# Optimization experiments

Hardware: AMD Instinct MI355X
Metric: run time of the kernel (lower is better)

The kernel has to match this reference:

```python
import jax, jax.numpy as jnp
import numpy as np

V, C, L, D = 16384, 16, 6, 64  # n_vars, max_clauses, max_variables, embedding_dim


def _normalize(x):
    # utils.normalize: L2-normalize along the feature axis
    return x / jnp.linalg.norm(x, axis=-1, keepdims=True)


def _rescombine(x, W1, b1, W2, b2):
    # ResidualCombine: normalize(sigmoid(layer1(x)) + layer2(x))
    h = jax.nn.sigmoid(x @ W1 + b1) + x @ W2 + b2
    return _normalize(h)


def setup_inputs() -> dict:
    key = jax.random.key(0)
    ks = jax.random.split(key, 14)
    s = 0.05
    variables = jax.random.normal(ks[0], (V, D), jnp.float32)
    # literal variable indices; slot 0 of every clause is the owning variable i
    lits = jax.random.randint(ks[1], (V, C, L), 0, V)
    lits = lits.at[:, :, 0].set(jnp.arange(V)[:, None])
    neg_mask = jax.random.bernoulli(ks[2], 0.5, (V, C, L))
    # literal validity: at least 2 literals per clause, slot 0 always valid
    nvar = jax.random.randint(ks[3], (V, C), 2, L + 1)
    var_valid = jnp.arange(L)[None, None, :] < nvar[:, :, None]
    # clause validity: at least 1 clause per variable
    nclause = jax.random.randint(ks[4], (V,), 1, C + 1)
    clause_valid = jnp.arange(C)[None, :] < nclause[:, None]
    # params
    Wn = jax.random.normal(ks[5], (D, D), jnp.float32) * s
    bn = jnp.zeros((D,), jnp.float32)
    f = jax.random.normal(ks[6], (D,), jnp.float32)
    false_emb = f / jnp.linalg.norm(f)  # Embedding(1, D, max_norm=1.0)
    W1v = jax.random.normal(ks[7], (L * D, D), jnp.float32) * s
    b1v = jnp.zeros((D,), jnp.float32)
    W2v = jax.random.normal(ks[8], (L * D, D), jnp.float32) * s
    b2v = jnp.zeros((D,), jnp.float32)
    W1c = jax.random.normal(ks[9], (C * D, D), jnp.float32) * s
    b1c = jnp.zeros((D,), jnp.float32)
    W2c = jax.random.normal(ks[10], (C * D, D), jnp.float32) * s
    b2c = jnp.zeros((D,), jnp.float32)
    return dict(variables=variables, lits=lits, neg_mask=neg_mask, var_valid=var_valid,
                clause_valid=clause_valid, Wn=Wn, bn=bn, false_emb=false_emb,
                W1v=W1v, b1v=b1v, W2v=W2v, b2v=b2v, W1c=W1c, b1c=b1c, W2c=W2c, b2c=b2c)


def reference(variables, lits, neg_mask, var_valid, clause_valid,
              Wn, bn, false_emb, W1v, b1v, W2v, b2v, W1c, b1c, W2c, b2c):
    # gather literal embeddings: [V, C, L, D]
    g = variables[lits]
    # negation linear for negative literals
    v = jnp.where(neg_mask[..., None], g @ Wn + bn, g)
    # pad invalid literal slots with the 'false' embedding
    v = jnp.where(var_valid[..., None], v, false_emb)
    # variable_combiner over flattened [L*D]
    clause_emb = _rescombine(v.reshape(V, C, L * D), W1v, b1v, W2v, b2v)  # [V, C, D]
    # pad missing clauses with 'true' = negation(false)
    true_emb = false_emb @ Wn + bn
    clause_emb = jnp.where(clause_valid[..., None], clause_emb, true_emb)
    # clause_combiner over flattened [C*D]
    out = _rescombine(clause_emb.reshape(V, C * D), W1c, b1c, W2c, b2c)  # [V, D]
    # variables with no clauses pass through unchanged
    has_clauses = clause_valid.any(axis=-1)
    return jnp.where(has_clauses[:, None], out, variables)
```

## Files before the change

### kernel.cpp

```cpp
#include <hip/hip_runtime.h>
#include <hip/hip_bf16.h>

#define NV 16384
#define NC 16
#define NL 6
#define ND 64

typedef unsigned short u16;
typedef unsigned int u32;
typedef __attribute__((ext_vector_type(8))) short short8;
typedef __attribute__((ext_vector_type(4))) float f32x4;

#define PB_BN  0
#define PB_FE  64
#define PB_B1V 128
#define PB_B2V 192
#define PB_B1C 256
#define PB_B2C 320
#define U_BVS   896
#define U_BCS   50048
#define U_VARSB 185216
#define U_NEGB  1233856
#define U_FIDX  2282496

__device__ __forceinline__ float ldbf(const u16* p, int i) {
  return __uint_as_float(((u32)p[i]) << 16);
}
__device__ __forceinline__ u16 f2b(float f) {
  u32 x = __float_as_uint(f);
  return (u16)((x + 0x7FFF + ((x >> 16) & 1)) >> 16);
}
__device__ __forceinline__ int ldmask(const void* p, int i, int bdt) {
  return bdt ? (int)((const signed char*)p)[i] : ((const int*)p)[i];
}
__device__ __forceinline__ float ldf(const void* p, int i, int fdt) {
  return fdt ? ldbf((const u16*)p, i) : ((const float*)p)[i];
}
__device__ __forceinline__ void gll16(const u16* g, u16* l) {
  __builtin_amdgcn_global_load_lds(
      (const __attribute__((address_space(1))) u32*)(g),
      (__attribute__((address_space(3))) u32*)(l), 16, 0, 0);
}

__global__ __launch_bounds__(256) void k_prep(
    const void* vars, const int* __restrict__ lits, const void* negm, const void* vval,
    const void* Wn, const void* bn, const void* femb,
    const void* W1v, const void* b1v, const void* W2v, const void* b2v,
    const void* W1c, const void* b1c, const void* W2c, const void* b2c,
    int* flags, float* pbuf, u16* wsB) {
  __shared__ int s_cnt[4], s_big[4];
  __shared__ __align__(16) u16 BnL[4096];
  const int t = threadIdx.x;
  {
    const u32 w = ((const u32*)vars)[t];
    const u32 e = (w >> 7) & 0xFF;
    const unsigned long long bal = __ballot(e >= 0x6E && e <= 0x8E);
    const u32 bw = ((const u32*)vval)[t];
    const unsigned long long bb = __ballot(bw > 1u);
    if ((t & 63) == 0) { s_cnt[t >> 6] = __popcll(bal); s_big[t >> 6] = (bb != 0ull); }
  }
  __syncthreads();
  const int fdt = (s_cnt[0] + s_cnt[1] + s_cnt[2] + s_cnt[3]) >= 192;
  const int bdt = (s_big[0] | s_big[1] | s_big[2] | s_big[3]);
  const int bid = blockIdx.x;

  if (bid == 0) {
    if (t == 0) { flags[0] = fdt; flags[1] = bdt; }
    if (t < 64) {
      const void* src[6] = {bn, femb, b1v, b2v, b1c, b2c};
      const int off[6] = {PB_BN, PB_FE, PB_B1V, PB_B2V, PB_B1C, PB_B2C};
      for (int j = 0; j < 6; j++) pbuf[off[j] + t] = ldf(src[j], t, fdt);
      wsB[U_VARSB + NV * 64 + t] = fdt ? ((const u16*)femb)[t] : f2b(((const float*)femb)[t]);
    }
  } else if (bid < 25) {
    const int c = (bid - 1) * 256 + t;
    const int ln = c & 63, nt = (c >> 6) & 7, ks = c >> 9;
    const int n = nt * 16 + (ln & 15);
    const void* src = (n < 64) ? W1v : W2v;
    const int kb = ks * 32 + (ln >> 4) * 8, n6 = n & 63;
    u16 o[8];
#pragma unroll
    for (int j = 0; j < 8; j++) o[j] = f2b(ldf(src, (kb + j) * 64 + n6, fdt));
    *(short8*)(wsB + U_BVS + c * 8) = *(short8*)o;
  } else if (bid < 89) {
    const int c = (bid - 25) * 256 + t;
    const int ln = c & 63, nt = (c >> 6) & 7, ks = c >> 9;
    const int n = nt * 16 + (ln & 15);
    const void* src = (n < 64) ? W1c : W2c;
    const int kb = ks * 32 + (ln >> 4) * 8, n6 = n & 63;
    u16 o[8];
#pragma unroll
    for (int j = 0; j < 8; j++) o[j] = f2b(ldf(src, (kb + j) * 64 + n6, fdt));
    *(short8*)(wsB + U_BCS + c * 8) = *(short8*)o;
  } else if (bid < 217) {
    const int c8 = ((bid - 89) * 256 + t) * 4;
#pragma unroll
    for (int cc = 0; cc < 4; cc++) {
      u16 o[8];
      if (fdt) {
        *(short8*)o = ((const short8*)vars)[c8 + cc];
      } else {
        const float* f = (const float*)vars + (c8 + cc) * 8;
#pragma unroll
        for (int j = 0; j < 8; j++) o[j] = f2b(f[j]);
      }
      *(short8*)(wsB + U_VARSB + (c8 + cc) * 8) = *(short8*)o;
    }
  } else if (bid < 601) {
    const int i0 = ((bid - 217) * 256 + t) * 16;
    u16 o[16];
    if (!bdt) {
      const int4* lp = (const int4*)(lits + i0);
      const int4* vp = (const int4*)((const int*)vval + i0);
      const int4* np = (const int4*)((const int*)negm + i0);
#pragma unroll
      for (int c4 = 0; c4 < 4; c4++) {
        const int4 L = lp[c4], V = vp[c4], N = np[c4];
        o[c4 * 4 + 0] = (u16)(V.x ? (L.x + (N.x ? (NV + 1) : 0)) : NV);
        o[c4 * 4 + 1] = (u16)(V.y ? (L.y + (N.y ? (NV + 1) : 0)) : NV);
        o[c4 * 4 + 2] = (u16)(V.z ? (L.z + (N.z ? (NV + 1) : 0)) : NV);
        o[c4 * 4 + 3] = (u16)(V.w ? (L.w + (N.w ? (NV + 1) : 0)) : NV);
      }
    } else {
#pragma unroll
      for (int j = 0; j < 16; j++) {
        const int i = i0 + j;
        const int valid = ldmask(vval, i, bdt);
        const int neg = ldmask(negm, i, bdt);
        o[j] = (u16)(valid ? (lits[i] + (neg ? (NV + 1) : 0)) : NV);
      }
    }
    *(short8*)(wsB + U_FIDX + i0) = *(short8*)o;
    *(short8*)(wsB + U_FIDX + i0 + 8) = *(short8*)(o + 8);
  } else {
    const int lane = t & 63, wv = t >> 6;
    const int col = lane & 15, quad = lane >> 4, q8 = quad * 8;
    const int rowbase = (bid - 601) * 64 + wv * 16;
    for (int i = t; i < 4096; i += 256) {
      const int n = i >> 6, k = i & 63;
      BnL[i] = f2b(ldf(Wn, k * 64 + n, fdt));
    }
    __syncthreads();
    const int arow = min(rowbase + col, NV);
    short8 a[2];
    if (fdt) {
      const u16* src = (arow == NV) ? (const u16*)femb : (const u16*)vars + arow * 64;
      a[0] = *(const short8*)(src + q8);
      a[1] = *(const short8*)(src + 32 + q8);
    } else {
      const float* src = (arow == NV) ? (const float*)femb : (const float*)vars + arow * 64;
      u16 tmp[16];
#pragma unroll
      for (int j = 0; j < 8; j++) tmp[j] = f2b(src[q8 + j]);
#pragma unroll
      for (int j = 0; j < 8; j++) tmp[8 + j] = f2b(src[32 + q8 + j]);
      a[0] = *(short8*)tmp;
      a[1] = *(short8*)(tmp + 8);
    }
    f32x4 acc[4];
#pragma unroll
    for (int nt = 0; nt < 4; nt++) acc[nt] = (f32x4){0.f, 0.f, 0.f, 0.f};
#pragma unroll
    for (int ks = 0; ks < 2; ks++) {
#pragma unroll
      for (int nt = 0; nt < 4; nt++) {
        const short8 b = *(const short8*)(BnL + (nt * 16 + col) * 64 + ks * 32 + q8);
        acc[nt] = __builtin_amdgcn_mfma_f32_16x16x32_bf16(a[ks], b, acc[nt], 0, 0, 0);
      }
    }
#pragma unroll
    for (int reg = 0; reg < 4; reg++) {
      const int r = rowbase + quad * 4 + reg;
      if (r <= NV) {
#pragma unroll
        for (int nt = 0; nt < 4; nt++) {
          const int d = nt * 16 + col;
          wsB[U_NEGB + r * 64 + d] = f2b(acc[nt][reg] + ldf(bn, d, fdt));
        }
      }
    }
  }
}

__global__ __launch_bounds__(256, 2) void k_main(
    const void* __restrict__ vars, const void* __restrict__ cval,
    const float* __restrict__ pbuf, const int* __restrict__ flags,
    const u16* __restrict__ wsB, void* __restrict__ outv) {
  __shared__ __align__(16) u16 smem[24576];
  __shared__ float ps[16][4];
  __shared__ int hcS[16];

  const int tid = threadIdx.x, lane = tid & 63, wv = tid >> 6;
  const int col = lane & 15, quad = lane >> 4, q8 = quad * 8;
  const int fdt = flags[0], bdt = flags[1];
  const int vbase = (blockIdx.x * 4 + wv) * 4;
  const int v0 = blockIdx.x * 16;

  u32 r2_[4][3];
#pragma unroll
  for (int v4 = 0; v4 < 4; v4++)
#pragma unroll
    for (int i = 0; i < 3; i++)
      r2_[v4][i] = *(const u32*)(wsB + U_FIDX + (vbase + v4) * 96 + col * 6 + i * 2);

  const int cv = ldmask(cval, vbase * 16 + lane, bdt);
  const unsigned long long bal = __ballot(cv != 0);
  if (lane < 4) hcS[wv * 4 + lane] = ((bal >> (lane * 16)) & 0xFFFFull) != 0;

  f32x4 acc[4][8];
#pragma unroll
  for (int v4 = 0; v4 < 4; v4++)
#pragma unroll
    for (int nt = 0; nt < 8; nt++) acc[v4][nt] = (f32x4){0.f, 0.f, 0.f, 0.f};

#pragma unroll
  for (int j = 0; j < 6; j++) {
    const int cl = wv * 6 + j;
    gll16(wsB + U_BVS + cl * 512 + lane * 8, &smem[cl * 512]);
  }
  short8 a_cur[4], a_nxt[4];
#pragma unroll
  for (int v4 = 0; v4 < 4; v4++) {
    const int idx = (int)(r2_[v4][0] & 0xFFFFu);
    a_cur[v4] = *(const short8*)(wsB + U_VARSB + idx * 64 + q8);
  }
  __syncthreads();

  for (int q = 0; q < 4; q++) {
    if (q < 3) {
#pragma unroll
      for (int j = 0; j < 6; j++) {
        const int cl = wv * 6 + j;
        gll16(wsB + U_BVS + (q + 1) * 12288 + cl * 512 + lane * 8,
              &smem[((q + 1) & 1) * 12288 + cl * 512]);
      }
    }
#pragma unroll
    for (int ksl = 0; ksl < 3; ksl++) {
      const int gk = q * 3 + ksl;
      if (gk < 11) {
        const int gn = gk + 1;
        const int goff = (gn & 1) * 32 + q8;
        const int pi = gn >> 2, ph = (gn >> 1) & 1;
#pragma unroll
        for (int v4 = 0; v4 < 4; v4++) {
          const int idx = (int)((r2_[v4][pi] >> (ph * 16)) & 0xFFFFu);
          a_nxt[v4] = *(const short8*)(wsB + U_VARSB + idx * 64 + goff);
        }
      }
#pragma unroll
      for (int nt = 0; nt < 8; nt++) {
        const short8 b = *(const short8*)(&smem[(q & 1) * 12288 + (ksl * 8 + nt) * 512 + lane * 8]);
#pragma unroll
        for (int v4 = 0; v4 < 4; v4++)
          acc[v4][nt] = __builtin_amdgcn_mfma_f32_16x16x32_bf16(a_cur[v4], b, acc[v4][nt], 0, 0, 0);
      }
#pragma unroll
      for (int v4 = 0; v4 < 4; v4++) a_cur[v4] = a_nxt[v4];
    }
    if (q < 3) __syncthreads();
  }
  __syncthreads();

  {
    float b1l[4], b2l[4], truel[4];
#pragma unroll
    for (int nt = 0; nt < 4; nt++) {
      const int d = nt * 16 + col;
      b1l[nt] = pbuf[PB_B1V + d];
      b2l[nt] = pbuf[PB_B2V + d];
      truel[nt] = ldbf(wsB, U_NEGB + NV * 64 + d);
    }
#pragma unroll
    for (int v4 = 0; v4 < 4; v4++) {
      const u32 vmask = (u32)((bal >> (v4 * 16)) & 0xFFFFull);
      const int vloc = wv * 4 + v4;
#pragma unroll
      for (int reg = 0; reg < 4; reg++) {
        const int c = quad * 4 + reg;
        float hh[4], ss = 0.f;
#pragma unroll
        for (int nt = 0; nt < 4; nt++) {
          hh[nt] = 1.0f / (1.0f + __expf(-(acc[v4][nt][reg] + b1l[nt]))) + acc[v4][nt + 4][reg] + b2l[nt];
          ss += hh[nt] * hh[nt];
        }
        ss += __shfl_xor(ss, 1, 64); ss += __shfl_xor(ss, 2, 64);
        ss += __shfl_xor(ss, 4, 64); ss += __shfl_xor(ss, 8, 64);
        const float sc = 1.0f / sqrtf(ss);
        const int valid = (vmask >> c) & 1;
#pragma unroll
        for (int nt = 0; nt < 4; nt++) {
          const float o = valid ? hh[nt] * sc : truel[nt];
          const int l2 = (nt * 2 + (col >> 3)) & 3;
          smem[(c * 2 + (nt >> 1)) * 512 + (l2 * 16 + vloc) * 8 + (col & 7)] = f2b(o);
        }
      }
    }
  }
  __syncthreads();

  f32x4 acc1 = (f32x4){0.f, 0.f, 0.f, 0.f}, acc2 = (f32x4){0.f, 0.f, 0.f, 0.f};
#pragma unroll 8
  for (int ks = 0; ks < 32; ks++) {
    const short8 a = *(const short8*)(&smem[ks * 512 + lane * 8]);
    const short8 b1 = *(const short8*)(wsB + U_BCS + (ks * 8 + wv) * 512 + lane * 8);
    const short8 b2 = *(const short8*)(wsB + U_BCS + (ks * 8 + wv + 4) * 512 + lane * 8);
    acc1 = __builtin_amdgcn_mfma_f32_16x16x32_bf16(a, b1, acc1, 0, 0, 0);
    acc2 = __builtin_amdgcn_mfma_f32_16x16x32_bf16(a, b2, acc2, 0, 0, 0);
  }

  const int d = wv * 16 + col;
  const float b1c_d = pbuf[PB_B1C + d], b2c_d = pbuf[PB_B2C + d];
  float h[4];
#pragma unroll
  for (int reg = 0; reg < 4; reg++) {
    h[reg] = 1.0f / (1.0f + __expf(-(acc1[reg] + b1c_d))) + acc2[reg] + b2c_d;
    float ssp = h[reg] * h[reg];
    ssp += __shfl_xor(ssp, 1, 64); ssp += __shfl_xor(ssp, 2, 64);
    ssp += __shfl_xor(ssp, 4, 64); ssp += __shfl_xor(ssp, 8, 64);
    if (col == 0) ps[quad * 4 + reg][wv] = ssp;
  }
  __syncthreads();
#pragma unroll
  for (int reg = 0; reg < 4; reg++) {
    const int r = quad * 4 + reg;
    const float tot = ps[r][0] + ps[r][1] + ps[r][2] + ps[r][3];
    float o = h[reg] * (1.0f / sqrtf(tot));
    const int oi = (v0 + r) * 64 + d;
    if (hcS[r]) {
      if (fdt) ((u16*)outv)[oi] = f2b(o);
      else ((float*)outv)[oi] = o;
    } else {
      if (fdt) ((u16*)outv)[oi] = ((const u16*)vars)[oi];
      else ((float*)outv)[oi] = ((const float*)vars)[oi];
    }
  }
}

extern "C" void kernel_launch(void* const* d_in, const int* in_sizes, int n_in,
                              void* d_out, int out_size, void* d_ws, size_t ws_size,
                              hipStream_t stream) {
  const void* vars = d_in[0];
  const int* lits = (const int*)d_in[1];
  const void* negm = d_in[2];
  const void* vval = d_in[3];
  const void* cvalid = d_in[4];
  const void* Wn = d_in[5];
  const void* bn = d_in[6];
  const void* femb = d_in[7];
  const void* W1v = d_in[8];
  const void* b1v = d_in[9];
  const void* W2v = d_in[10];
  const void* b2v = d_in[11];
  const void* W1c = d_in[12];
  const void* b1c = d_in[13];
  const void* W2c = d_in[14];
  const void* b2c = d_in[15];

  int* flags = (int*)d_ws;
  float* pbuf = (float*)((char*)d_ws + 256);
  u16* wsB = (u16*)d_ws;

  k_prep<<<858, 256, 0, stream>>>(vars, lits, negm, vval, Wn, bn, femb,
                                  W1v, b1v, W2v, b2v, W1c, b1c, W2c, b2c,
                                  flags, pbuf, wsB);
  k_main<<<NV / 16, 256, 0, stream>>>(vars, cvalid, pbuf, flags, wsB, d_out);
}
```

Baseline: 159.4 us.

## Double k_main block to 32 variables with 8 waves and reuse clause weights

```diff
diff --git a/kernel.cpp b/kernel.cpp
--- a/kernel.cpp
+++ b/kernel.cpp
@@ -75,9 +75,9 @@
   } else if (bid < 25) {
     const int c = (bid - 1) * 256 + t;
     const int ln = c & 63, nt = (c >> 6) & 7, ks = c >> 9;
-    const int n = nt * 16 + (ln & 15);
-    const void* src = (n < 64) ? W1v : W2v;
-    const int kb = ks * 32 + (ln >> 4) * 8, n6 = n & 63;
+    const void* src = (nt < 4) ? W1v : W2v;
+    const int n6 = (ln & 15) * 4 + (nt & 3);
+    const int kb = ks * 32 + (ln >> 4) * 8;
     u16 o[8];
 #pragma unroll
     for (int j = 0; j < 8; j++) o[j] = f2b(ldf(src, (kb + j) * 64 + n6, fdt));
@@ -182,19 +182,19 @@
   }
 }
 
-__global__ __launch_bounds__(256, 2) void k_main(
+__global__ __launch_bounds__(512, 1) void k_main(
     const void* __restrict__ vars, const void* __restrict__ cval,
     const float* __restrict__ pbuf, const int* __restrict__ flags,
     const u16* __restrict__ wsB, void* __restrict__ outv) {
-  __shared__ __align__(16) u16 smem[24576];
-  __shared__ float ps[16][4];
-  __shared__ int hcS[16];
+  __shared__ __align__(16) u16 smem[32768];
+  __shared__ float ps[32][4];
+  __shared__ int hcS[32];
 
   const int tid = threadIdx.x, lane = tid & 63, wv = tid >> 6;
   const int col = lane & 15, quad = lane >> 4, q8 = quad * 8;
   const int fdt = flags[0], bdt = flags[1];
-  const int vbase = (blockIdx.x * 4 + wv) * 4;
-  const int v0 = blockIdx.x * 16;
+  const int vbase = blockIdx.x * 32 + wv * 4;
+  const int v0 = blockIdx.x * 32;
 
   u32 r2_[4][3];
 #pragma unroll
@@ -214,8 +214,8 @@
     for (int nt = 0; nt < 8; nt++) acc[v4][nt] = (f32x4){0.f, 0.f, 0.f, 0.f};
 
 #pragma unroll
-  for (int j = 0; j < 6; j++) {
-    const int cl = wv * 6 + j;
+  for (int j = 0; j < 3; j++) {
+    const int cl = wv * 3 + j;
     gll16(wsB + U_BVS + cl * 512 + lane * 8, &smem[cl * 512]);
   }
   short8 a_cur[4], a_nxt[4];
@@ -229,8 +229,8 @@
   for (int q = 0; q < 4; q++) {
     if (q < 3) {
 #pragma unroll
-      for (int j = 0; j < 6; j++) {
-        const int cl = wv * 6 + j;
+      for (int j = 0; j < 3; j++) {
+        const int cl = wv * 3 + j;
         gll16(wsB + U_BVS + (q + 1) * 12288 + cl * 512 + lane * 8,
               &smem[((q + 1) & 1) * 12288 + cl * 512]);
       }
@@ -263,76 +263,95 @@
   __syncthreads();
 
   {
-    float b1l[4], b2l[4], truel[4];
-#pragma unroll
-    for (int nt = 0; nt < 4; nt++) {
-      const int d = nt * 16 + col;
-      b1l[nt] = pbuf[PB_B1V + d];
-      b2l[nt] = pbuf[PB_B2V + d];
-      truel[nt] = ldbf(wsB, U_NEGB + NV * 64 + d);
-    }
+    const float4 b1l = *(const float4*)(pbuf + PB_B1V + col * 4);
+    const float4 b2l = *(const float4*)(pbuf + PB_B2V + col * 4);
+    float truel[4];
+#pragma unroll
+    for (int jj = 0; jj < 4; jj++) truel[jj] = ldbf(wsB, U_NEGB + NV * 64 + col * 4 + jj);
+    const int grp = wv >> 2;
+    const int vloc = (wv & 3) * 4;
 #pragma unroll
     for (int v4 = 0; v4 < 4; v4++) {
       const u32 vmask = (u32)((bal >> (v4 * 16)) & 0xFFFFull);
-      const int vloc = wv * 4 + v4;
 #pragma unroll
       for (int reg = 0; reg < 4; reg++) {
         const int c = quad * 4 + reg;
         float hh[4], ss = 0.f;
-#pragma unroll
-        for (int nt = 0; nt < 4; nt++) {
-          hh[nt] = 1.0f / (1.0f + __expf(-(acc[v4][nt][reg] + b1l[nt]))) + acc[v4][nt + 4][reg] + b2l[nt];
-          ss += hh[nt] * hh[nt];
-        }
+        hh[0] = 1.0f / (1.0f + __expf(-(acc[v4][0][reg] + b1l.x))) + acc[v4][4][reg] + b2l.x;
+        hh[1] = 1.0f / (1.0f + __expf(-(acc[v4][1][reg] + b1l.y))) + acc[v4][5][reg] + b2l.y;
+        hh[2] = 1.0f / (1.0f + __expf(-(acc[v4][2][reg] + b1l.z))) + acc[v4][6][reg] + b2l.z;
+        hh[3] = 1.0f / (1.0f + __expf(-(acc[v4][3][reg] + b1l.w))) + acc[v4][7][reg] + b2l.w;
+#pragma unroll
+        for (int jj = 0; jj < 4; jj++) ss += hh[jj] * hh[jj];
         ss += __shfl_xor(ss, 1, 64); ss += __shfl_xor(ss, 2, 64);
         ss += __shfl_xor(ss, 4, 64); ss += __shfl_xor(ss, 8, 64);
-        const float sc = 1.0f / sqrtf(ss);
+        const float sc = rsqrtf(ss);
         const int valid = (vmask >> c) & 1;
-#pragma unroll
-        for (int nt = 0; nt < 4; nt++) {
-          const float o = valid ? hh[nt] * sc : truel[nt];
-          const int l2 = (nt * 2 + (col >> 3)) & 3;
-          smem[(c * 2 + (nt >> 1)) * 512 + (l2 * 16 + vloc) * 8 + (col & 7)] = f2b(o);
+        ushort4 pk;
+        pk.x = f2b(valid ? hh[0] * sc : truel[0]);
+        pk.y = f2b(valid ? hh[1] * sc : truel[1]);
+        pk.z = f2b(valid ? hh[2] * sc : truel[2]);
+        pk.w = f2b(valid ? hh[3] * sc : truel[3]);
+        const int addr = grp * 16384 + (c * 2 + (col >> 3)) * 512 +
+                         (((col >> 1) & 3) * 16 + vloc + v4) * 8 + (col & 1) * 4;
+        *(ushort4*)(&smem[addr]) = pk;
+      }
+    }
+  }
+  __syncthreads();
+
+  float h0[4], h1[4];
+  if (wv < 4) {
+    const int nq = wv;
+    f32x4 a00 = (f32x4){0.f, 0.f, 0.f, 0.f}, a01 = a00, a10 = a00, a11 = a00;
+#pragma unroll 8
+    for (int ks = 0; ks < 32; ks++) {
+      const short8 a0 = *(const short8*)(&smem[ks * 512 + lane * 8]);
+      const short8 a1 = *(const short8*)(&smem[16384 + ks * 512 + lane * 8]);
+      const short8 b1 = *(const short8*)(wsB + U_BCS + (ks * 8 + nq) * 512 + lane * 8);
+      const short8 b2 = *(const short8*)(wsB + U_BCS + (ks * 8 + nq + 4) * 512 + lane * 8);
+      a00 = __builtin_amdgcn_mfma_f32_16x16x32_bf16(a0, b1, a00, 0, 0, 0);
+      a01 = __builtin_amdgcn_mfma_f32_16x16x32_bf16(a0, b2, a01, 0, 0, 0);
+      a10 = __builtin_amdgcn_mfma_f32_16x16x32_bf16(a1, b1, a10, 0, 0, 0);
+      a11 = __builtin_amdgcn_mfma_f32_16x16x32_bf16(a1, b2, a11, 0, 0, 0);
+    }
+    const int d = nq * 16 + col;
+    const float b1c_d = pbuf[PB_B1C + d], b2c_d = pbuf[PB_B2C + d];
+#pragma unroll
+    for (int reg = 0; reg < 4; reg++) {
+      h0[reg] = 1.0f / (1.0f + __expf(-(a00[reg] + b1c_d))) + a01[reg] + b2c_d;
+      h1[reg] = 1.0f / (1.0f + __expf(-(a10[reg] + b1c_d))) + a11[reg] + b2c_d;
+      float s0 = h0[reg] * h0[reg], s1 = h1[reg] * h1[reg];
+      s0 += __shfl_xor(s0, 1, 64); s0 += __shfl_xor(s0, 2, 64);
+      s0 += __shfl_xor(s0, 4, 64); s0 += __shfl_xor(s0, 8, 64);
+      s1 += __shfl_xor(s1, 1, 64); s1 += __shfl_xor(s1, 2, 64);
+      s1 += __shfl_xor(s1, 4, 64); s1 += __shfl_xor(s1, 8, 64);
+      if (col == 0) {
+        ps[quad * 4 + reg][nq] = s0;
+        ps[16 + quad * 4 + reg][nq] = s1;
+      }
+    }
+  }
+  __syncthreads();
+  if (wv < 4) {
+    const int d = wv * 16 + col;
+#pragma unroll
+    for (int reg = 0; reg < 4; reg++) {
+#pragma unroll
+      for (int g = 0; g < 2; g++) {
+        const int r = g * 16 + quad * 4 + reg;
+        const float tot = ps[r][0] + ps[r][1] + ps[r][2] + ps[r][3];
+        const float hv = g ? h1[reg] : h0[reg];
+        float o = hv * rsqrtf(tot);
+        const int oi = (v0 + r) * 64 + d;
+        if (hcS[r]) {
+          if (fdt) ((u16*)outv)[oi] = f2b(o);
+          else ((float*)outv)[oi] = o;
+        } else {
+          if (fdt) ((u16*)outv)[oi] = ((const u16*)vars)[oi];
+          else ((float*)outv)[oi] = ((const float*)vars)[oi];
         }
       }
-    }
-  }
-  __syncthreads();
-
-  f32x4 acc1 = (f32x4){0.f, 0.f, 0.f, 0.f}, acc2 = (f32x4){0.f, 0.f, 0.f, 0.f};
-#pragma unroll 8
-  for (int ks = 0; ks < 32; ks++) {
-    const short8 a = *(const short8*)(&smem[ks * 512 + lane * 8]);
-    const short8 b1 = *(const short8*)(wsB + U_BCS + (ks * 8 + wv) * 512 + lane * 8);
-    const short8 b2 = *(const short8*)(wsB + U_BCS + (ks * 8 + wv + 4) * 512 + lane * 8);
-    acc1 = __builtin_amdgcn_mfma_f32_16x16x32_bf16(a, b1, acc1, 0, 0, 0);
-    acc2 = __builtin_amdgcn_mfma_f32_16x16x32_bf16(a, b2, acc2, 0, 0, 0);
-  }
-
-  const int d = wv * 16 + col;
-  const float b1c_d = pbuf[PB_B1C + d], b2c_d = pbuf[PB_B2C + d];
-  float h[4];
-#pragma unroll
-  for (int reg = 0; reg < 4; reg++) {
-    h[reg] = 1.0f / (1.0f + __expf(-(acc1[reg] + b1c_d))) + acc2[reg] + b2c_d;
-    float ssp = h[reg] * h[reg];
-    ssp += __shfl_xor(ssp, 1, 64); ssp += __shfl_xor(ssp, 2, 64);
-    ssp += __shfl_xor(ssp, 4, 64); ssp += __shfl_xor(ssp, 8, 64);
-    if (col == 0) ps[quad * 4 + reg][wv] = ssp;
-  }
-  __syncthreads();
-#pragma unroll
-  for (int reg = 0; reg < 4; reg++) {
-    const int r = quad * 4 + reg;
-    const float tot = ps[r][0] + ps[r][1] + ps[r][2] + ps[r][3];
-    float o = h[reg] * (1.0f / sqrtf(tot));
-    const int oi = (v0 + r) * 64 + d;
-    if (hcS[r]) {
-      if (fdt) ((u16*)outv)[oi] = f2b(o);
-      else ((float*)outv)[oi] = o;
-    } else {
-      if (fdt) ((u16*)outv)[oi] = ((const u16*)vars)[oi];
-      else ((float*)outv)[oi] = ((const float*)vars)[oi];
     }
   }
 }
@@ -364,5 +383,5 @@
   k_prep<<<858, 256, 0, stream>>>(vars, lits, negm, vval, Wn, bn, femb,
                                   W1v, b1v, W2v, b2v, W1c, b1c, W2c, b2c,
                                   flags, pbuf, wsB);
-  k_main<<<NV / 16, 256, 0, stream>>>(vars, cvalid, pbuf, flags, wsB, d_out);
-}
+  k_main<<<NV / 32, 512, 0, stream>>>(vars, cvalid, pbuf, flags, wsB, d_out);
+}
```

New measurement: 169.3 us. +6.2%, slower.
